# Kernel tuning notes

Hardware: AMD Instinct MI355X
Metric: run time of the kernel (lower is better)

Reference implementation:

```python
import jax, jax.numpy as jnp
import numpy as np

# ---- dopri5 (RK45) tableau ----
C2, C3, C4, C5 = 1/5, 3/10, 4/5, 8/9
A21 = 1/5
A31, A32 = 3/40, 9/40
A41, A42, A43 = 44/45, -56/15, 32/9
A51, A52, A53, A54 = 19372/6561, -25360/2187, 64448/6561, -212/729
A61, A62, A63, A64, A65 = 9017/3168, -355/33, 46732/5247, 49/176, -5103/18656
B1, B3, B4, B5, B6 = 35/384, 500/1113, 125/192, -2187/6784, 11/84
# error coefficients = b(5th) - b(4th)
E1, E3, E4, E5, E6, E7 = 71/57600, -71/16695, 71/1920, -17253/339200, 22/525, -1/40

N_STEPS = 24          # fixed scan length for the adaptive loop (jit-friendly)
RTOL = ATOL = 1e-3    # tolerance from init_kwargs
DT0 = 0.1             # initial step size


def conv_time(t, x, w, b, padding):
    # append time as an extra channel, then NCHW conv
    t_img = jnp.full_like(x[:, :1], t)
    xt = jnp.concatenate([t_img, x], axis=1)
    y = jax.lax.conv_general_dilated(xt, w, (1, 1), padding,
                                     dimension_numbers=('NCHW', 'OIHW', 'NCHW'))
    return y + b[None, :, None, None]


def ode_func(t, x, w1, b1, w2, b2, w3, b3):
    h = jax.nn.relu(conv_time(t, x, w1, b1, [(0, 0), (0, 0)]))
    h = jax.nn.relu(conv_time(t, h, w2, b2, [(1, 1), (1, 1)]))
    return conv_time(t, h, w3, b3, [(0, 0), (0, 0)])


def dopri5_step(f, t, y, dt):
    k1 = f(t, y)
    k2 = f(t + dt * C2, y + dt * (A21 * k1))
    k3 = f(t + dt * C3, y + dt * (A31 * k1 + A32 * k2))
    k4 = f(t + dt * C4, y + dt * (A41 * k1 + A42 * k2 + A43 * k3))
    k5 = f(t + dt * C5, y + dt * (A51 * k1 + A52 * k2 + A53 * k3 + A54 * k4))
    k6 = f(t + dt, y + dt * (A61 * k1 + A62 * k2 + A63 * k3 + A64 * k4 + A65 * k5))
    y5 = y + dt * (B1 * k1 + B3 * k3 + B4 * k4 + B5 * k5 + B6 * k6)
    k7 = f(t + dt, y5)  # FSAL stage, used for error estimate
    err = dt * (E1 * k1 + E3 * k3 + E4 * k4 + E5 * k5 + E6 * k6 + E7 * k7)
    return y5, err


def integrate(f, y0):
    """Adaptive dopri5 from t=0 to t=1 with fixed-length masked scan."""
    def step(carry, _):
        t, y, dt = carry
        dt_c = jnp.minimum(dt, 1.0 - t)
        y_new, err = dopri5_step(f, t, y, dt_c)
        tol = ATOL + RTOL * jnp.maximum(jnp.abs(y), jnp.abs(y_new))
        err_norm = jnp.sqrt(jnp.mean((err / tol) ** 2))
        done = t >= 1.0 - 1e-7
        adv = (err_norm <= 1.0) & (~done)
        t_n = jnp.where(adv, t + dt_c, t)
        y_n = jnp.where(adv, y_new, y)
        safe = jnp.maximum(err_norm, 1e-10)
        factor = jnp.clip(0.9 * safe ** (-0.2), 0.2, 10.0)
        dt_n = jnp.where(done, dt, dt_c * factor)
        return (t_n, y_n, dt_n), None

    step = jax.checkpoint(step)
    (t, y, dt), _ = jax.lax.scan(step,
                                 (jnp.float32(0.0), y0, jnp.float32(DT0)),
                                 None, length=N_STEPS)
    return y


def setup_inputs() -> dict:
    key = jax.random.key(0)
    ks = jax.random.split(key, 9)
    B, Cin, H, W = 64, 3, 32, 32
    AUG, NF = 5, 64
    CH = Cin + AUG  # 8
    x = jax.random.normal(ks[0], (B, Cin, H, W), dtype=jnp.float32)
    def wgt(k, shape):
        fan_in = shape[1] * shape[2] * shape[3]
        return jax.random.normal(k, shape, dtype=jnp.float32) / np.sqrt(fan_in).astype(np.float32)
    w1 = wgt(ks[1], (NF, CH + 1, 1, 1)); b1 = jnp.zeros((NF,), jnp.float32)
    w2 = wgt(ks[2], (NF, NF + 1, 3, 3)); b2 = jnp.zeros((NF,), jnp.float32)
    w3 = wgt(ks[3], (CH, NF + 1, 1, 1)); b3 = jnp.zeros((CH,), jnp.float32)
    flat = CH * H * W  # 8192
    wl = jax.random.normal(ks[4], (10, flat), dtype=jnp.float32) / np.sqrt(flat).astype(np.float32)
    bl = jnp.zeros((10,), jnp.float32)
    return {"x": x, "w1": w1, "b1": b1, "w2": w2, "b2": b2,
            "w3": w3, "b3": b3, "wl": wl, "bl": bl}


def reference(x, w1, b1, w2, b2, w3, b3, wl, bl):
    B, C, H, W = x.shape
    AUG = w3.shape[0] - C  # augmented channels
    aug = jnp.zeros((B, AUG, H, W), dtype=x.dtype)
    y0 = jnp.concatenate([x, aug], axis=1)
    f = lambda t, y: ode_func(t, y, w1, b1, w2, b2, w3, b3)
    yT = integrate(f, y0)                    # state at t = 1
    out = yT.reshape(B, -1) @ wl.T + bl      # final linear head
    return out
```

## Files before the change

kernel.cpp:

```cpp
#include <hip/hip_runtime.h>
#include <math.h>

namespace {
constexpr int BN = 64;
constexpr int HW = 1024;
constexpr int NS = BN*8*HW;

constexpr float C2f = 0.2f, C3f = 0.3f, C4f = 0.8f, C5f = (float)(8.0/9.0);
constexpr float A21 = 0.2f;
constexpr float A31 = (float)(3.0/40.0),  A32 = (float)(9.0/40.0);
constexpr float A41 = (float)(44.0/45.0), A42 = (float)(-56.0/15.0), A43 = (float)(32.0/9.0);
constexpr float A51 = (float)(19372.0/6561.0), A52 = (float)(-25360.0/2187.0),
                A53 = (float)(64448.0/6561.0), A54 = (float)(-212.0/729.0);
constexpr float A61 = (float)(9017.0/3168.0), A62 = (float)(-355.0/33.0),
                A63 = (float)(46732.0/5247.0), A64 = (float)(49.0/176.0),
                A65 = (float)(-5103.0/18656.0);
constexpr float B1c = (float)(35.0/384.0), B3c = (float)(500.0/1113.0),
                B4c = (float)(125.0/192.0), B5c = (float)(-2187.0/6784.0),
                B6c = (float)(11.0/84.0);
constexpr float E1c = (float)(71.0/57600.0), E3c = (float)(-71.0/16695.0),
                E4c = (float)(71.0/1920.0), E5c = (float)(-17253.0/339200.0),
                E6c = (float)(22.0/525.0),  E7c = (float)(-1.0/40.0);
constexpr float RTOL = 1e-3f, ATOL = 1e-3f;

constexpr size_t OFF_PART = 0;
constexpr size_t OFF_FLAG = 1024;
constexpr size_t OFF_CNT  = 1536;
constexpr size_t OFF_TSUM = 1600;
constexpr size_t OFF_W2P  = 2176;
constexpr size_t OFF_Y    = 20608;
constexpr size_t OFF_Y5   = OFF_Y  + (size_t)NS;
constexpr size_t OFF_K    = OFF_Y5 + (size_t)NS;
constexpr size_t OFF_WPK  = OFF_K + (size_t)7*NS;
}

__constant__ float g_cf[6][5] = {
    {A21, 0, 0, 0, 0},
    {A31, A32, 0, 0, 0},
    {A41, A42, A43, 0, 0},
    {A51, A52, A53, A54, 0},
    {A61, A62, A63, A64, A65},
    {0, 0, 0, 0, 0}};
__constant__ float g_ct[6] = {C2f, C3f, C4f, C5f, 1.0f, 1.0f};

typedef _Float16 hfrag8 __attribute__((ext_vector_type(8)));
typedef float f32x16 __attribute__((ext_vector_type(16)));

__device__ __forceinline__ float ld_sysf(const float* p) {
    return __hip_atomic_load(p, __ATOMIC_RELAXED, __HIP_MEMORY_SCOPE_SYSTEM);
}
__device__ __forceinline__ float2 ld_sysf2(const float* p) {
    union { unsigned long long u; float2 f; } c;
    c.u = __hip_atomic_load((const unsigned long long*)p, __ATOMIC_RELAXED,
                            __HIP_MEMORY_SCOPE_SYSTEM);
    return c.f;
}
__device__ __forceinline__ void st_sysf(float* p, float v) {
    __hip_atomic_store(p, v, __ATOMIC_RELAXED, __HIP_MEMORY_SCOPE_SYSTEM);
}
__device__ __forceinline__ void st_sysf2(float* p, float a, float b) {
    union { unsigned long long u; float2 f; } c;
    c.f = make_float2(a, b);
    __hip_atomic_store((unsigned long long*)p, c.u, __ATOMIC_RELAXED,
                       __HIP_MEMORY_SCOPE_SYSTEM);
}

__device__ __forceinline__ void ld8(const float* p, float* v, bool sys) {
    if (sys) {
        #pragma unroll
        for (int h = 0; h < 4; h++) {
            float2 t = ld_sysf2(p + 2*h);
            v[2*h] = t.x; v[2*h+1] = t.y;
        }
    } else {
        float4 a = *(const float4*)p;
        float4 b = *(const float4*)(p + 4);
        v[0]=a.x; v[1]=a.y; v[2]=a.z; v[3]=a.w;
        v[4]=b.x; v[5]=b.y; v[6]=b.z; v[7]=b.w;
    }
}
__device__ __forceinline__ void st8(float* p, const float* v, bool sys) {
    if (sys) {
        st_sysf2(p,     v[0], v[1]);
        st_sysf2(p + 2, v[2], v[3]);
        st_sysf2(p + 4, v[4], v[5]);
        st_sysf2(p + 6, v[6], v[7]);
    } else {
        *(float4*)p       = make_float4(v[0], v[1], v[2], v[3]);
        *(float4*)(p + 4) = make_float4(v[4], v[5], v[6], v[7]);
    }
}

__global__ __launch_bounds__(256)
void k_init(const float* __restrict__ x, float* __restrict__ y,
            int* __restrict__ flags, unsigned* __restrict__ cnt)
{
    int idx = blockIdx.x*256 + threadIdx.x;
    int b = idx >> 13, px = (idx >> 3) & 1023, c = idx & 7;
    y[idx] = (c < 3) ? x[(size_t)(b*3 + c)*1024 + px] : 0.0f;
    if (idx < 512) flags[idx] = 0;
    if (idx == 600) *cnt = 0u;
}

__global__ __launch_bounds__(256)
void k_prepack(const float* __restrict__ w1, const float* __restrict__ w2,
               const float* __restrict__ w3, _Float16* __restrict__ w2p,
               float* __restrict__ tsum, float* __restrict__ wpk)
{
    int gid = blockIdx.x*256 + threadIdx.x;
    if (gid < 36864) {
        int j    = gid & 7;
        int lane = (gid >> 3) & 63;
        int nt   = (gid >> 9) & 1;
        int ks   = (gid >> 10) & 3;
        int tap  = gid >> 12;
        int oc = nt*32 + (lane & 31);
        int ic = ks*16 + (lane >> 5)*8 + j;
        w2p[gid] = (_Float16)w2[oc*585 + (1 + ic)*9 + tap];
    }
    if (gid < 576) {
        int oc = gid & 63, combo = gid >> 6;
        int rcase = combo / 3, ccase = combo % 3;
        float s = 0.0f;
        for (int kh = 0; kh < 3; kh++) {
            if ((rcase == 1 && kh == 0) || (rcase == 2 && kh == 2)) continue;
            for (int kw = 0; kw < 3; kw++) {
                if ((ccase == 1 && kw == 0) || (ccase == 2 && kw == 2)) continue;
                s += w2[oc*585 + kh*3 + kw];
            }
        }
        tsum[gid] = s;
    }
    if (gid < 512) wpk[gid] = w1[(gid & 63)*9 + 1 + (gid >> 6)];
    if (gid < 64)  wpk[512 + gid] = w1[gid*9];
    if (gid < 512) wpk[576 + gid] = w3[(gid & 7)*65 + 1 + (gid >> 3)];
    if (gid < 8)   wpk[1088 + gid] = w3[gid*65];
}

__global__ void __launch_bounds__(256, 2)
k_ode(const float* __restrict__ b1, const float* __restrict__ b2,
      const float* __restrict__ b3, const _Float16* __restrict__ w2p,
      const float* __restrict__ tsumg, const float* __restrict__ wpk,
      const float* __restrict__ wl, const float* __restrict__ bl,
      float* __restrict__ ybuf, float* __restrict__ y5buf,
      float* __restrict__ kb, float* __restrict__ part,
      int* __restrict__ flags, float* __restrict__ out)
{
    __shared__ __align__(16) unsigned char s_pool[55488];
    __shared__ __align__(16) _Float16 s_z[1552];
    __shared__ float s_tsum[576];
    __shared__ float s_b2v[64], s_b1v[64], s_w10v[64];
    __shared__ float s_w30v[8], s_b3v[8];
    __shared__ float s_red[256];

    const int tid = threadIdx.x;
    const int nblk = gridDim.x;
    const int lane = tid & 63;
    const int m32 = lane & 31, q2 = lane >> 5;
    const int rp = tid >> 7;
    const int np = (tid >> 6) & 1;
    const int wid = tid >> 6;

    if (tid < 64) {
        s_b2v[tid] = b2[tid];
        s_b1v[tid] = b1[tid];
        s_w10v[tid] = wpk[512 + tid];
    }
    if (tid < 8) { s_w30v[tid] = wpk[1088 + tid]; s_b3v[tid] = b3[tid]; }
    for (int i = tid; i < 576; i += 256) s_tsum[i] = tsumg[i];
    if (tid < 8) s_z[192*8 + tid] = (_Float16)0.0f;
    __syncthreads();

    const int oct1 = wid >> 1;
    hfrag8 w1f;
    #pragma unroll
    for (int j = 0; j < 8; j++)
        w1f[j] = q2 ? (_Float16)0.0f : (_Float16)wpk[j*64 + oct1*32 + m32];
    hfrag8 w3f[4];
    #pragma unroll
    for (int kst = 0; kst < 4; kst++)
        #pragma unroll
        for (int j = 0; j < 8; j++) {
            int ch = kst*16 + q2*8 + j;
            w3f[kst][j] = (m32 < 8) ? (_Float16)wpk[576 + ch*8 + m32]
                                    : (_Float16)0.0f;
        }

    float t = 0.0f, dt = 0.1f;
    float* ya = ybuf; float* yb = y5buf;
    float* ka = kb;  float* kg = kb + 6*(size_t)NS;

    auto wait_all = [&](int target) {
        for (;;) {
            bool ok = (__hip_atomic_load(&flags[tid], __ATOMIC_RELAXED,
                           __HIP_MEMORY_SCOPE_SYSTEM) >= target)
                   && (__hip_atomic_load(&flags[tid + 256], __ATOMIC_RELAXED,
                           __HIP_MEMORY_SCOPE_SYSTEM) >= target);
            if (__syncthreads_and((int)ok)) break;
            __builtin_amdgcn_s_sleep(2);
        }
    };

    auto eval = [&](const float* src, int nc, const float* cf, float ctv,
                    float* kout, int mode, int gev, float* partp) {
        float dtc = fminf(dt, 1.0f - t);
        float ts  = t + ctv*dtc;

        for (int tile = blockIdx.x; tile < 512; tile += nblk) {
            int b = tile >> 3, rg = tile & 7;

            if (tid < 96) {
                int px_id = tid >> 3, u = tid & 7;
                int row = px_id >> 1, colh = (px_id & 1) ? 33 : 0;
                *(uint4*)(s_pool + (size_t)(row*34 + colh)*272 + u*16) =
                    make_uint4(0u,0u,0u,0u);
            }

            if (tid < 192) {
                int w = tid >> 5;
                int lr = (0x504132 >> (4*w)) & 7;
                int col = tid & 31;
                int r = rg*4 - 1 + lr;
                bool sysrow = (lr < 2) | (lr > 3);
                if (gev > 1 && w >= 4) {
                    const int* fp = (lr == 0) ? &flags[tile-1] : &flags[tile+1];
                    bool need = (lr == 0) ? (rg > 0) : (rg < 7);
                    while (need && __hip_atomic_load(fp, __ATOMIC_RELAXED,
                                                     __HIP_MEMORY_SCOPE_SYSTEM) < gev-1)
                        __builtin_amdgcn_s_sleep(1);
                }
                union { _Float16 h[8]; uint4 u; } pz;
                if ((unsigned)r < 32u) {
                    int px = (r << 5) + col;
                    size_t pb8 = ((size_t)(b << 10) + px) << 3;
                    float kv[5][8], sv[8];
                    if (sysrow) {
                        #pragma unroll
                        for (int j = 0; j < 5; j++) if (j < nc) {
                            const float* kp = (j == 0 ? ka : kb + (size_t)j*NS) + pb8;
                            #pragma unroll
                            for (int h = 0; h < 4; h++) {
                                float2 t2 = ld_sysf2(kp + 2*h);
                                kv[j][2*h] = t2.x; kv[j][2*h+1] = t2.y;
                            }
                        }
                        #pragma unroll
                        for (int h = 0; h < 4; h++) {
                            float2 t2 = ld_sysf2(src + pb8 + 2*h);
                            sv[2*h] = t2.x; sv[2*h+1] = t2.y;
                        }
                    } else {
                        #pragma unroll
                        for (int j = 0; j < 5; j++) if (j < nc) {
                            const float* kp = (j == 0 ? ka : kb + (size_t)j*NS) + pb8;
                            float4 a4 = *(const float4*)kp;
                            float4 b4 = *(const float4*)(kp + 4);
                            kv[j][0]=a4.x; kv[j][1]=a4.y; kv[j][2]=a4.z; kv[j][3]=a4.w;
                            kv[j][4]=b4.x; kv[j][5]=b4.y; kv[j][6]=b4.z; kv[j][7]=b4.w;
                        }
                        float4 a4 = *(const float4*)(src + pb8);
                        float4 b4 = *(const float4*)(src + pb8 + 4);
                        sv[0]=a4.x; sv[1]=a4.y; sv[2]=a4.z; sv[3]=a4.w;
                        sv[4]=b4.x; sv[5]=b4.y; sv[6]=b4.z; sv[7]=b4.w;
                    }
                    float s[8] = {0,0,0,0,0,0,0,0};
                    #pragma unroll
                    for (int j = 0; j < 5; j++) if (j < nc) {
                        float a = cf[j];
                        #pragma unroll
                        for (int c = 0; c < 8; c++) s[c] = fmaf(a, kv[j][c], s[c]);
                    }
                    #pragma unroll
                    for (int c = 0; c < 8; c++)
                        pz.h[c] = (_Float16)(sv[c] + dtc*s[c]);
                } else {
                    pz.u = make_uint4(0u,0u,0u,0u);
                }
                *(uint4*)(s_z + (size_t)(lr*32 + col)*8) = pz.u;
            }
            __syncthreads();

            {
                int pgbase = (wid & 1)*3;
                #pragma unroll
                for (int i = 0; i < 3; i++) {
                    int pxg = pgbase + i;
                    int r = rg*4 - 1 + pxg;
                    bool valid = ((unsigned)r < 32u);
                    const _Float16* zp = s_z + (q2 ? (size_t)192*8
                                                   : (size_t)(pxg*32 + m32)*8);
                    hfrag8 bz = *(const hfrag8*)zp;
                    f32x16 a1 = (f32x16)(0.0f);
                    a1 = __builtin_amdgcn_mfma_f32_32x32x16_f16(w1f, bz, a1, 0,0,0);
                    unsigned words[8];
                    #pragma unroll
                    for (int pr = 0; pr < 8; pr++) {
                        int r0 = 2*pr;
                        int oc0 = oct1*32 + (r0&3) + 8*(r0>>2) + 4*q2;
                        float v0 = valid ? fmaxf(a1[r0]   + ts*s_w10v[oc0]
                                                 + s_b1v[oc0],   0.0f) : 0.0f;
                        float v1 = valid ? fmaxf(a1[r0+1] + ts*s_w10v[oc0+1]
                                                 + s_b1v[oc0+1], 0.0f) : 0.0f;
                        union { _Float16 h[2]; unsigned u; } pk;
                        pk.h[0] = (_Float16)v0; pk.h[1] = (_Float16)v1;
                        words[pr] = pk.u;
                    }
                    unsigned char* basep = s_pool
                        + (size_t)(pxg*34 + m32 + 1)*272 + oct1*64 + q2*8;
                    #pragma unroll
                    for (int wq = 0; wq < 4; wq++)
                        *(uint2*)(basep + wq*16) =
                            make_uint2(words[2*wq], words[2*wq+1]);
                }
            }
            __syncthreads();

            f32x16 acc2[2];
            acc2[0] = (f32x16)(0.0f);
            acc2[1] = (f32x16)(0.0f);
            for (int cc = 0; cc < 2; cc++) {
                #pragma unroll 1
                for (int kh = 0; kh < 3; kh++) {
                    #pragma unroll
                    for (int kw = 0; kw < 3; kw++) {
                        int tap = kh*3 + kw;
                        #pragma unroll
                        for (int s = 0; s < 2; s++) {
                            int ks = cc*2 + s;
                            hfrag8 aw = *(const hfrag8*)
                                (w2p + (size_t)((tap*4 + ks)*2 + np)*512 + lane*8);
                            int aoff = ks*32 + q2*16;
                            #pragma unroll
                            for (int ri = 0; ri < 2; ri++) {
                                int lr = rp*2 + ri + kh;
                                hfrag8 bact = *(const hfrag8*)(s_pool
                                    + (size_t)(lr*34 + m32 + kw)*272 + aoff);
                                acc2[ri] = __builtin_amdgcn_mfma_f32_32x32x16_f16(
                                    aw, bact, acc2[ri], 0, 0, 0);
                            }
                        }
                    }
                }
            }
            __syncthreads();

            {
                int ccase = (m32 == 0) ? 1 : ((m32 == 31) ? 2 : 0);
                #pragma unroll
                for (int ri = 0; ri < 2; ri++) {
                    int pg = rp*2 + ri;
                    int r_out = rg*4 + pg;
                    int rcase = (r_out == 0) ? 1 : ((r_out == 31) ? 2 : 0);
                    const float* tsb = &s_tsum[(rcase*3 + ccase)*64];
                    int px = pg*32 + m32;
                    unsigned words[8];
                    #pragma unroll
                    for (int pr = 0; pr < 8; pr++) {
                        int r0 = 2*pr;
                        int oc0 = np*32 + (r0&3) + 8*(r0>>2) + 4*q2;
                        float v0 = fmaxf(acc2[ri][r0]   + ts*tsb[oc0]
                                         + s_b2v[oc0],   0.0f);
                        float v1 = fmaxf(acc2[ri][r0+1] + ts*tsb[oc0+1]
                                         + s_b2v[oc0+1], 0.0f);
                        union { _Float16 h[2]; unsigned u; } pk;
                        pk.h[0] = (_Float16)v0; pk.h[1] = (_Float16)v1;
                        words[pr] = pk.u;
                    }
                    unsigned char* basep = s_pool + (size_t)px*144
                                           + np*64 + q2*8;
                    #pragma unroll
                    for (int wq = 0; wq < 4; wq++)
                        *(uint2*)(basep + wq*16) =
                            make_uint2(words[2*wq], words[2*wq+1]);
                }
            }
            __syncthreads();

            {
                f32x16 a3a = (f32x16)(0.0f);
                const unsigned char* hb = (const unsigned char*)s_pool;
                #pragma unroll
                for (int kst = 0; kst < 4; kst++) {
                    hfrag8 bh2 = *(const hfrag8*)(hb
                        + (size_t)(wid*32 + m32)*144 + kst*32 + q2*16);
                    a3a = __builtin_amdgcn_mfma_f32_32x32x16_f16(
                        w3f[kst], bh2, a3a, 0, 0, 0);
                }
                float a3[8];
                #pragma unroll
                for (int r = 0; r < 4; r++) {
                    float own = a3a[r];
                    float oth = __shfl(own, lane ^ 32, 64);
                    a3[r]     = q2 ? oth : own;
                    a3[4 + r] = q2 ? own : oth;
                }
                float ls = 0.0f;
                if (q2 == 0) {
                    #pragma unroll
                    for (int c = 0; c < 8; c++)
                        a3[c] += fmaf(ts, s_w30v[c], s_b3v[c]);
                    bool sysrow = (wid == 0) | (wid == 3);
                    int px = rg*128 + wid*32 + m32;
                    size_t pb8 = ((size_t)(b << 10) + px) << 3;
                    st8(kout + pb8, a3, sysrow);
                    if (mode == 1) {
                        float kv1[8], kv3[8], kv4[8], kv5[8], yv[8], r8[8];
                        ld8(ka + pb8, kv1, sysrow);
                        ld8(kb + 2*(size_t)NS + pb8, kv3, sysrow);
                        ld8(kb + 3*(size_t)NS + pb8, kv4, sysrow);
                        ld8(kb + 4*(size_t)NS + pb8, kv5, sysrow);
                        ld8(ya + pb8, yv, sysrow);
                        #pragma unroll
                        for (int c = 0; c < 8; c++)
                            r8[c] = yv[c] + dtc*(B1c*kv1[c] + B3c*kv3[c]
                                    + B4c*kv4[c] + B5c*kv5[c] + B6c*a3[c]);
                        st8(yb + pb8, r8, sysrow);
                    } else if (mode == 2) {
                        float kv1[8], kv3[8], kv4[8], kv5[8], kv6[8], yv[8], y5v[8];
                        ld8(ka + pb8, kv1, sysrow);
                        ld8(kb + 2*(size_t)NS + pb8, kv3, sysrow);
                        ld8(kb + 3*(size_t)NS + pb8, kv4, sysrow);
                        ld8(kb + 4*(size_t)NS + pb8, kv5, sysrow);
                        ld8(kb + 5*(size_t)NS + pb8, kv6, sysrow);
                        ld8(ya + pb8, yv, sysrow);
                        ld8(yb + pb8, y5v, sysrow);
                        #pragma unroll
                        for (int c = 0; c < 8; c++) {
                            float e = dtc*(E1c*kv1[c] + E3c*kv3[c] + E4c*kv4[c]
                                           + E5c*kv5[c] + E6c*kv6[c] + E7c*a3[c]);
                            float tol = ATOL + RTOL*fmaxf(fabsf(yv[c]), fabsf(y5v[c]));
                            float rr = e / tol;
                            ls += rr*rr;
                        }
                    }
                }
                if (mode == 2) {
                    s_red[tid] = ls;
                    __syncthreads();
                    for (int sft = 128; sft > 0; sft >>= 1) {
                        if (tid < sft) s_red[tid] += s_red[tid + sft];
                        __syncthreads();
                    }
                    if (tid == 0) st_sysf(&partp[tile], s_red[0]);
                }
            }
            __syncthreads();
            if (tid == 0)
                __hip_atomic_store(&flags[tile], gev, __ATOMIC_RELAXED,
                                   __HIP_MEMORY_SCOPE_SYSTEM);
        }
    };

    int gev = 1;
    eval(ya, 0, g_cf[5], 0.0f, ka, 0, gev, part);
    gev++;

    for (int st = 0; st < 24; st++) {
        if (t >= 1.0f - 1e-7f) break;
        float* partp = part + (size_t)(st & 1)*512;
        for (int e = 0; e < 6; e++) {
            int nc = (e < 5) ? e + 1 : 0;
            const float* src = (e == 5) ? yb : ya;
            float* kout = (e < 5) ? kb + (size_t)(e + 1)*NS : kg;
            int mode = (e == 4) ? 1 : ((e == 5) ? 2 : 0);
            eval(src, nc, g_cf[e], g_ct[e], kout, mode, gev, partp);
            gev++;
        }
        wait_all(gev - 1);
        float v = ld_sysf(&partp[tid]) + ld_sysf(&partp[tid + 256]);
        s_red[tid] = v;
        __syncthreads();
        for (int sft = 128; sft > 0; sft >>= 1) {
            if (tid < sft) s_red[tid] += s_red[tid + sft];
            __syncthreads();
        }
        float red0 = s_red[0];
        __syncthreads();
        float err_norm = sqrtf(red0 / (float)NS);
        float dtc = fminf(dt, 1.0f - t);
        bool adv = (err_norm <= 1.0f);
        if (adv) {
            t = t + dtc;
            float* tmp = ya; ya = yb; yb = tmp;
            tmp = ka; ka = kg; kg = tmp;
        }
        float safe = fmaxf(err_norm, 1e-10f);
        float factor = fminf(fmaxf(0.9f*powf(safe, -0.2f), 0.2f), 10.0f);
        dt = dtc*factor;
    }

    for (int tile = blockIdx.x; tile < 512; tile += nblk) {
        int b = tile >> 3, rg = tile & 7;
        if (tid < 128) {
            int lrow = tid >> 5;
            if (lrow == 1 || lrow == 2) {
                int px = rg*128 + tid;
                float* yp = ya + (((size_t)(b << 10) + px) << 3);
                float4 v0 = *(const float4*)yp;
                float4 v1 = *(const float4*)(yp + 4);
                st_sysf2(yp,     v0.x, v0.y);
                st_sysf2(yp + 2, v0.z, v0.w);
                st_sysf2(yp + 4, v1.x, v1.y);
                st_sysf2(yp + 6, v1.z, v1.w);
            }
        }
    }
    __syncthreads();
    for (int tile = blockIdx.x; tile < 512; tile += nblk)
        if (tid == 0)
            __hip_atomic_store(&flags[tile], gev, __ATOMIC_RELAXED,
                               __HIP_MEMORY_SCOPE_SYSTEM);
    wait_all(gev);

    for (int bh = blockIdx.x; bh < 64; bh += nblk) {
        float* s_hred = (float*)s_pool;
        float acc[10];
        #pragma unroll
        for (int m = 0; m < 10; m++) acc[m] = 0.0f;
        for (int px = tid; px < 1024; px += 256) {
            const float* yp = ya + (((size_t)(bh << 10) + px) << 3);
            float yv[8];
            #pragma unroll
            for (int h = 0; h < 4; h++) {
                float2 v = ld_sysf2(yp + 2*h);
                yv[2*h] = v.x; yv[2*h+1] = v.y;
            }
            #pragma unroll
            for (int c = 0; c < 8; c++) {
                float v = yv[c];
                #pragma unroll
                for (int m = 0; m < 10; m++)
                    acc[m] = fmaf(v, wl[(size_t)m*8192 + (c << 10) + px], acc[m]);
            }
        }
        #pragma unroll
        for (int m = 0; m < 10; m++) s_hred[m*256 + tid] = acc[m];
        __syncthreads();
        for (int sft = 128; sft > 0; sft >>= 1) {
            if (tid < sft) {
                #pragma unroll
                for (int m = 0; m < 10; m++)
                    s_hred[m*256 + tid] += s_hred[m*256 + tid + sft];
            }
            __syncthreads();
        }
        if (tid < 10) out[bh*10 + tid] = s_hred[tid*256] + bl[tid];
        __syncthreads();
    }
}

extern "C" void kernel_launch(void* const* d_in, const int* in_sizes, int n_in,
                              void* d_out, int out_size, void* d_ws, size_t ws_size,
                              hipStream_t stream)
{
    const float* x  = (const float*)d_in[0];
    const float* w1 = (const float*)d_in[1];
    const float* b1 = (const float*)d_in[2];
    const float* w2 = (const float*)d_in[3];
    const float* b2 = (const float*)d_in[4];
    const float* w3 = (const float*)d_in[5];
    const float* b3 = (const float*)d_in[6];
    const float* wl = (const float*)d_in[7];
    const float* bl = (const float*)d_in[8];
    float* out = (float*)d_out;

    float* F = (float*)d_ws;
    float* part = F + OFF_PART;
    int*   flags = (int*)(F + OFF_FLAG);
    unsigned* cnt = (unsigned*)(F + OFF_CNT);
    float* tsum = F + OFF_TSUM;
    _Float16* w2p = (_Float16*)(F + OFF_W2P);
    float* y    = F + OFF_Y;
    float* y5   = F + OFF_Y5;
    float* kbp  = F + OFF_K;
    float* wpk  = F + OFF_WPK;

    k_init<<<NS/256, 256, 0, stream>>>(x, y, flags, cnt);
    k_prepack<<<144, 256, 0, stream>>>(w1, w2, w3, w2p, tsum, wpk);

    int maxb = 0;
    if (hipOccupancyMaxActiveBlocksPerMultiprocessor(&maxb,
            reinterpret_cast<const void*>(k_ode), 256, 0) != hipSuccess || maxb < 1)
        maxb = 1;
    int cus = 256;
    {
        int dev = 0;
        hipGetDevice(&dev);
        hipDeviceProp_t prop;
        if (hipGetDeviceProperties(&prop, dev) == hipSuccess && prop.multiProcessorCount > 0)
            cus = prop.multiProcessorCount;
    }
    long cap = (long)maxb * (long)cus;
    int gridn = (int)((cap < 512) ? cap : 512);
    if (gridn < 16) gridn = 16;

    k_ode<<<gridn, 256, 0, stream>>>(b1, b2, b3, w2p, tsum, wpk, wl, bl,
                                     y, y5, kbp, part, flags, out);
}
```

Baseline: 474.1 us.

## Reuse conv3x3 activation fragments via DPP lane shifts and split h2 buffer

Restructures the 3x3 conv MFMA loop so that each K-slice loads the centre-column activation fragment once per row from LDS. The left and right horizontal taps are built with DPP row shifts (zeroing the edge lanes) instead of separate LDS reads. This removes the halo zeroing and the padded-column layout dependency, and changes the LDS strides to reduce bank conflicts. The second-layer output moves to its own LDS buffer, which drops a __syncthreads between the conv and its epilogue. The cost is more register pressure and a larger total shared memory footprint, which may reduce occupancy. The DPP shift must cross the 32-lane boundary correctly for the result to stay right.

```diff
diff --git a/kernel.cpp b/kernel.cpp
--- a/kernel.cpp
+++ b/kernel.cpp
@@ -32,6 +32,9 @@
 constexpr size_t OFF_Y5   = OFF_Y  + (size_t)NS;
 constexpr size_t OFF_K    = OFF_Y5 + (size_t)NS;
 constexpr size_t OFF_WPK  = OFF_K + (size_t)7*NS;
+
+constexpr int ACT_STRIDE = 264;
+constexpr int H2_STRIDE  = 136;
 }
 
 __constant__ float g_cf[6][5] = {
@@ -45,6 +48,8 @@
 
 typedef _Float16 hfrag8 __attribute__((ext_vector_type(8)));
 typedef float f32x16 __attribute__((ext_vector_type(16)));
+
+union HU { hfrag8 h; unsigned u[4]; };
 
 __device__ __forceinline__ float ld_sysf(const float* p) {
     return __hip_atomic_load(p, __ATOMIC_RELAXED, __HIP_MEMORY_SCOPE_SYSTEM);
@@ -146,7 +151,8 @@
       float* __restrict__ kb, float* __restrict__ part,
       int* __restrict__ flags, float* __restrict__ out)
 {
-    __shared__ __align__(16) unsigned char s_pool[55488];
+    __shared__ __align__(16) unsigned char s_pool[53600];
+    __shared__ __align__(16) unsigned char s_h2[17408];
     __shared__ __align__(16) _Float16 s_z[1552];
     __shared__ float s_tsum[576];
     __shared__ float s_b2v[64], s_b1v[64], s_w10v[64];
@@ -160,6 +166,8 @@
     const int rp = tid >> 7;
     const int np = (tid >> 6) & 1;
     const int wid = tid >> 6;
+    const bool lz32 = (lane == 32);
+    const bool lz31 = (lane == 31);
 
     if (tid < 64) {
         s_b2v[tid] = b2[tid];
@@ -209,13 +217,6 @@
         for (int tile = blockIdx.x; tile < 512; tile += nblk) {
             int b = tile >> 3, rg = tile & 7;
 
-            if (tid < 96) {
-                int px_id = tid >> 3, u = tid & 7;
-                int row = px_id >> 1, colh = (px_id & 1) ? 33 : 0;
-                *(uint4*)(s_pool + (size_t)(row*34 + colh)*272 + u*16) =
-                    make_uint4(0u,0u,0u,0u);
-            }
-
             if (tid < 192) {
                 int w = tid >> 5;
                 int lr = (0x504132 >> (4*w)) & 7;
@@ -306,7 +307,7 @@
                         words[pr] = pk.u;
                     }
                     unsigned char* basep = s_pool
-                        + (size_t)(pxg*34 + m32 + 1)*272 + oct1*64 + q2*8;
+                        + (size_t)(pxg*34 + m32 + 1)*ACT_STRIDE + oct1*64 + q2*8;
                     #pragma unroll
                     for (int wq = 0; wq < 4; wq++)
                         *(uint2*)(basep + wq*16) =
@@ -318,31 +319,50 @@
             f32x16 acc2[2];
             acc2[0] = (f32x16)(0.0f);
             acc2[1] = (f32x16)(0.0f);
-            for (int cc = 0; cc < 2; cc++) {
+            {
+                const unsigned char* actb = (const unsigned char*)s_pool;
                 #pragma unroll 1
-                for (int kh = 0; kh < 3; kh++) {
-                    #pragma unroll
-                    for (int kw = 0; kw < 3; kw++) {
-                        int tap = kh*3 + kw;
-                        #pragma unroll
-                        for (int s = 0; s < 2; s++) {
-                            int ks = cc*2 + s;
+                for (int ks = 0; ks < 4; ks++) {
+                    HU fc[4], d0[4], d2[4];
+                    #pragma unroll
+                    for (int l = 0; l < 4; l++) {
+                        const unsigned char* p = actb
+                            + (size_t)((rp*2 + l)*34 + m32 + 1)*ACT_STRIDE
+                            + ks*32 + q2*16;
+                        *(uint2*)&fc[l].u[0] = *(const uint2*)p;
+                        *(uint2*)&fc[l].u[2] = *(const uint2*)(p + 8);
+                    }
+                    #pragma unroll
+                    for (int l = 0; l < 4; l++) {
+                        #pragma unroll
+                        for (int i = 0; i < 4; i++) {
+                            unsigned s0 = (unsigned)__builtin_amdgcn_update_dpp(
+                                0, (int)fc[l].u[i], 0x138, 0xF, 0xF, true);
+                            d0[l].u[i] = lz32 ? 0u : s0;
+                            unsigned s2 = (unsigned)__builtin_amdgcn_update_dpp(
+                                0, (int)fc[l].u[i], 0x130, 0xF, 0xF, true);
+                            d2[l].u[i] = lz31 ? 0u : s2;
+                        }
+                    }
+                    #pragma unroll
+                    for (int kh = 0; kh < 3; kh++) {
+                        #pragma unroll
+                        for (int kw = 0; kw < 3; kw++) {
+                            int tap = kh*3 + kw;
                             hfrag8 aw = *(const hfrag8*)
                                 (w2p + (size_t)((tap*4 + ks)*2 + np)*512 + lane*8);
-                            int aoff = ks*32 + q2*16;
                             #pragma unroll
                             for (int ri = 0; ri < 2; ri++) {
-                                int lr = rp*2 + ri + kh;
-                                hfrag8 bact = *(const hfrag8*)(s_pool
-                                    + (size_t)(lr*34 + m32 + kw)*272 + aoff);
+                                int l = ri + kh;
+                                hfrag8 bf = (kw == 0) ? d0[l].h
+                                          : ((kw == 1) ? fc[l].h : d2[l].h);
                                 acc2[ri] = __builtin_amdgcn_mfma_f32_32x32x16_f16(
-                                    aw, bact, acc2[ri], 0, 0, 0);
+                                    aw, bf, acc2[ri], 0, 0, 0);
                             }
                         }
                     }
                 }
             }
-            __syncthreads();
 
             {
                 int ccase = (m32 == 0) ? 1 : ((m32 == 31) ? 2 : 0);
@@ -366,7 +386,7 @@
                         pk.h[0] = (_Float16)v0; pk.h[1] = (_Float16)v1;
                         words[pr] = pk.u;
                     }
-                    unsigned char* basep = s_pool + (size_t)px*144
+                    unsigned char* basep = s_h2 + (size_t)px*H2_STRIDE
                                            + np*64 + q2*8;
                     #pragma unroll
                     for (int wq = 0; wq < 4; wq++)
@@ -378,13 +398,16 @@
 
             {
                 f32x16 a3a = (f32x16)(0.0f);
-                const unsigned char* hb = (const unsigned char*)s_pool;
+                const unsigned char* hb = (const unsigned char*)s_h2;
                 #pragma unroll
                 for (int kst = 0; kst < 4; kst++) {
-                    hfrag8 bh2 = *(const hfrag8*)(hb
-                        + (size_t)(wid*32 + m32)*144 + kst*32 + q2*16);
+                    HU f;
+                    const unsigned char* p = hb
+                        + (size_t)(wid*32 + m32)*H2_STRIDE + kst*32 + q2*16;
+                    *(uint2*)&f.u[0] = *(const uint2*)p;
+                    *(uint2*)&f.u[2] = *(const uint2*)(p + 8);
                     a3a = __builtin_amdgcn_mfma_f32_32x32x16_f16(
-                        w3f[kst], bh2, a3a, 0, 0, 0);
+                        w3f[kst], f.h, a3a, 0, 0, 0);
                 }
                 float a3[8];
                 #pragma unroll
```

Result: faster. 464.4 us (-2.1%).
